# Kernel optimization log

Hardware: AMD Instinct MI355X
Metric: run time of the kernel (lower is better)

Reference implementation:

```python
import jax, jax.numpy as jnp
import numpy as np

# ---- static config (mirrors cfg) ----
B, N, K = 2, 8192, 40
FIRST_DL = 0.03
CONV_RADIUS = 2.5
DEFORM_RADIUS = 5.0
ARCH = ['simple', 'resnetb', 'resnetb_strided', 'resnetb', 'resnetb_strided', 'resnetb', 'nearest_upsample']
SENTINEL = N  # out-of-range support index (torch code uses N_spts_total; here per-batch padded slot count)
GRID = 4096   # voxel hash multiplier; coords stay < GRID for pts in [0,1], dl >= 0.06


def _ball_query_one(q, s, qmask, smask, radius):
    """Radius ball-query: K nearest supports within radius. q:[N,3] s:[M,3]."""
    d2 = jnp.sum((q[:, None, :] - s[None, :, :]) ** 2, axis=-1)          # [N,M]
    d2 = jnp.where(smask[None, :] & (d2 <= radius * radius), d2, jnp.inf)
    vals, idx = jax.lax.top_k(-d2, K)                                     # [N,K]
    idx = jnp.where(jnp.isfinite(vals) & qmask[:, None], idx, SENTINEL)
    return idx.astype(jnp.int32)


ball_query = jax.vmap(_ball_query_one, in_axes=(0, 0, 0, 0, None))


def _grid_subsample_one(pts, mask, dl):
    """Voxel-grid subsampling with unweighted average (padded to N rows)."""
    INT_MAX = jnp.iinfo(jnp.int32).max
    c = jnp.floor(pts / dl).astype(jnp.int32)                             # nonneg for pts in [0,1]
    key_v = (c[:, 0] * GRID + c[:, 1]) * GRID + c[:, 2]
    key_v = jnp.where(mask, key_v, INT_MAX)
    order = jnp.argsort(key_v)
    sk = key_v[order]
    sp = pts[order]
    new = jnp.concatenate([jnp.ones((1,), bool), sk[1:] != sk[:-1]])
    seg = jnp.cumsum(new) - 1                                             # segment id per sorted point
    sums = jax.ops.segment_sum(sp, seg, num_segments=N)                   # [N,3]
    cnt = jax.ops.segment_sum(jnp.ones((N,), pts.dtype), seg, num_segments=N)
    segkey = jax.ops.segment_max(sk, seg, num_segments=N)
    valid = (cnt > 0) & (segkey != INT_MAX)                               # invalid pads sort last
    means = jnp.where(valid[:, None], sums / jnp.maximum(cnt, 1.0)[:, None], 0.0)
    return means, valid, jnp.sum(valid).astype(jnp.int32)


grid_subsample = jax.vmap(_grid_subsample_one, in_axes=(0, 0, None))


def setup_inputs() -> dict:
    key = jax.random.key(0)
    pts = jax.random.uniform(key, (B, N, 3), dtype=jnp.float32)
    return {"pts": pts}


def reference(pts):
    pmask = jnp.ones((B, N), bool)
    lengths = jnp.full((B,), N, jnp.int32)
    points = pts
    r_normal = FIRST_DL * CONV_RADIUS
    layer_blocks = []
    out_points, out_neigh, out_pool, out_up, out_len = [], [], [], [], []
    for bi, block in enumerate(ARCH):
        if 'global' in block or 'upsample' in block:
            break
        if not ('pool' in block or 'strided' in block):
            layer_blocks.append(block)
            if bi < len(ARCH) - 1 and 'upsample' not in ARCH[bi + 1]:
                continue
        if layer_blocks:
            if any('deformable' in b for b in layer_blocks[:-1]):
                r = r_normal * DEFORM_RADIUS / CONV_RADIUS
            else:
                r = r_normal
            conv_i = ball_query(points, points, pmask, pmask, r)
        else:
            conv_i = jnp.full((B, N, K), SENTINEL, jnp.int32)
        if 'pool' in block or 'strided' in block:
            dl = 2 * r_normal / CONV_RADIUS
            pool_p, pool_m, pool_len = grid_subsample(points, pmask, dl)
            r = r_normal * DEFORM_RADIUS / CONV_RADIUS if 'deformable' in block else r_normal
            pool_i = ball_query(pool_p, points, pool_m, pmask, r)
            up_i = ball_query(points, pool_p, pmask, pool_m, 2 * r)
        else:
            pool_i = jnp.full((B, N, K), SENTINEL, jnp.int32)
            up_i = jnp.full((B, N, K), SENTINEL, jnp.int32)
            pool_p = jnp.zeros((B, N, 3), points.dtype)
            pool_m = jnp.zeros((B, N), bool)
            pool_len = jnp.zeros((B,), jnp.int32)
        out_points.append(points)
        out_neigh.append(conv_i)
        out_pool.append(pool_i)
        out_up.append(up_i)
        out_len.append(lengths)
        points, pmask, lengths = pool_p, pool_m, pool_len
        r_normal *= 2
        layer_blocks = []
    return (jnp.stack(out_points),   # [L,B,N,3] padded points per layer
            jnp.stack(out_neigh),    # [L,B,N,K] conv neighbor indices
            jnp.stack(out_pool),     # [L,B,N,K] pooling indices
            jnp.stack(out_up),       # [L,B,N,K] upsampling indices
            jnp.stack(out_len))      # [L,B]     valid lengths
```

## Files before the change

kernel.cpp:

```cpp
#include <hip/hip_runtime.h>

#define BB   2
#define NN   8192
#define KNN  40
#define SENT 8192
#define G0   17
#define G1   9
#define G0_3 (G0*G0*G0)
#define G1_3 (G1*G1*G1)

#define GA   13
#define GB   6
#define GC   3
#define GA_3 (GA*GA*GA)
#define GB_3 (GB*GB*GB)
#define GC_3 (GC*GC*GC)

typedef unsigned long long ull;
typedef unsigned int       u32;
typedef unsigned short     u16;

__device__ __forceinline__ float sqdist(float qx, float qy, float qz,
                                        float sx, float sy, float sz) {
    float dx = __fsub_rn(qx, sx);
    float dy = __fsub_rn(qy, sy);
    float dz = __fsub_rn(qz, sz);
    return __fadd_rn(__fadd_rn(__fmul_rn(dx, dx), __fmul_rn(dy, dy)),
                     __fmul_rn(dz, dz));
}

__device__ __forceinline__ int cell1(float p, float Gf, int G) {
    int c = (int)floorf(__fmul_rn(p, Gf));
    return min(max(c, 0), G - 1);
}
__device__ __forceinline__ int vcell1(float p, float dlf, int G) {
    int c = (int)floorf(__fdiv_rn(p, dlf));
    return min(max(c, 0), G - 1);
}

__device__ __forceinline__ ull shfl_u64(ull x, int src) {
    int lo = __shfl((int)(u32)x, src);
    int hi = __shfl((int)(u32)(x >> 32), src);
    return ((ull)(u32)hi << 32) | (ull)(u32)lo;
}
__device__ __forceinline__ ull shflxor_u64(ull x, int m) {
    int lo = __shfl_xor((int)(u32)x, m);
    int hi = __shfl_xor((int)(u32)(x >> 32), m);
    return ((ull)(u32)hi << 32) | (ull)(u32)lo;
}

__global__ void prep_kernel(const float* __restrict__ pts, float* __restrict__ dout) {
    const size_t PN = (size_t)BB * NN * 3;
    const size_t IN = (size_t)BB * NN * KNN;
    float* out_points0 = dout;
    float* out_pool2   = dout + 3 * PN + 3 * IN + 2 * IN;
    float* out_up2     = dout + 3 * PN + 6 * IN + 2 * IN;
    float* out_len     = dout + 3 * PN + 9 * IN;
    int i = blockIdx.x * 256 + threadIdx.x;
    if (i < (int)PN) out_points0[i] = pts[i];
    if (i < (int)IN) {
        out_pool2[i] = (float)SENT;
        out_up2[i]   = (float)SENT;
    }
    if (i == 0) { out_len[0] = (float)NN; out_len[1] = (float)NN; }
}

__global__ __launch_bounds__(1024) void csr_build(
    const float* __restrict__ pts, const int* __restrict__ len_ptr, int len_const,
    int G, int G3, int* __restrict__ off, int* __restrict__ lst,
    float dlfv, int Gv, int G3v, int* __restrict__ offv, int* __restrict__ rankv,
    int* __restrict__ lstv, int* __restrict__ lenv_dev, float* __restrict__ lenv_out_f) {
    __shared__ int scnt[GA_3];
    __shared__ int soff[GA_3];
    __shared__ int svcnt[G0_3];
    __shared__ int svoff[G0_3];
    __shared__ int wsum[16];
    int b = blockIdx.x;
    int t = threadIdx.x;
    int len = len_ptr ? len_ptr[b] : len_const;
    const float* pb = pts + (size_t)b * NN * 3;
    float Gf = (float)G;
    bool dosub = Gv > 0;
    for (int v = t; v < G3; v += 1024) scnt[v] = 0;
    if (dosub) for (int v = t; v < G3v; v += 1024) svcnt[v] = 0;
    __syncthreads();
    for (int i = t; i < len; i += 1024) {
        float px = pb[i * 3], py = pb[i * 3 + 1], pz = pb[i * 3 + 2];
        int c = (cell1(px, Gf, G) * G + cell1(py, Gf, G)) * G + cell1(pz, Gf, G);
        atomicAdd(&scnt[c], 1);
        if (dosub) {
            int cv = (vcell1(px, dlfv, Gv) * Gv + vcell1(py, dlfv, Gv)) * Gv
                     + vcell1(pz, dlfv, Gv);
            atomicAdd(&svcnt[cv], 1);
        }
    }
    __syncthreads();
    int lane = t & 63, wid = t >> 6;
    {
        int per = (G3 + 1023) >> 10;
        int start = t * per, end = min(start + per, G3);
        if (start > G3) start = G3;
        int csum = 0;
        for (int v = start; v < end; ++v) csum += scnt[v];
        int inc = csum;
        for (int d = 1; d < 64; d <<= 1) {
            int u = __shfl_up(inc, d);
            if (lane >= d) inc += u;
        }
        if (lane == 63) wsum[wid] = inc;
        __syncthreads();
        if (t < 16) {
            int wv = wsum[t];
            for (int d = 1; d < 16; d <<= 1) {
                int u = __shfl_up(wv, d);
                if (t >= d) wv += u;
            }
            wsum[t] = wv;
        }
        __syncthreads();
        int excl = inc - csum + (wid ? wsum[wid - 1] : 0);
        int run = excl;
        int* offb = off + (size_t)b * (G3 + 1);
        for (int v = start; v < end; ++v) {
            soff[v] = run;
            offb[v] = run;
            run += scnt[v];
        }
        if (t == 0) offb[G3] = len;
    }
    __syncthreads();
    if (dosub) {
        int per = (G3v + 1023) >> 10;
        int start = t * per, end = min(start + per, G3v);
        if (start > G3v) start = G3v;
        int ce = 0, co = 0;
        for (int v = start; v < end; ++v) { ce += svcnt[v]; co += (svcnt[v] > 0); }
        int pack = (ce << 14) | co;
        int inc = pack;
        for (int d = 1; d < 64; d <<= 1) {
            int u = __shfl_up(inc, d);
            if (lane >= d) inc += u;
        }
        if (lane == 63) wsum[wid] = inc;
        __syncthreads();
        if (t < 16) {
            int wv = wsum[t];
            for (int d = 1; d < 16; d <<= 1) {
                int u = __shfl_up(wv, d);
                if (t >= d) wv += u;
            }
            wsum[t] = wv;
        }
        __syncthreads();
        int excl = inc - pack + (wid ? wsum[wid - 1] : 0);
        int rune = excl >> 14;
        int runo = excl & 16383;
        int total = wsum[15] & 16383;
        int* offvb  = offv  + (size_t)b * (G3v + 1);
        int* rankvb = rankv + (size_t)b * G3v;
        for (int v = start; v < end; ++v) {
            svoff[v]  = rune;
            offvb[v]  = rune;
            rankvb[v] = runo;
            rune += svcnt[v];
            runo += (svcnt[v] > 0);
        }
        if (t == 0) {
            offvb[G3v] = len;
            lenv_dev[b] = total;
            lenv_out_f[b] = (float)total;
        }
    }
    __syncthreads();
    for (int v = t; v < G3; v += 1024) scnt[v] = 0;
    if (dosub) for (int v = t; v < G3v; v += 1024) svcnt[v] = 0;
    __syncthreads();
    int* lstb = lst + (size_t)b * NN;
    int* lstvb = dosub ? (lstv + (size_t)b * NN) : nullptr;
    for (int i = t; i < len; i += 1024) {
        float px = pb[i * 3], py = pb[i * 3 + 1], pz = pb[i * 3 + 2];
        int c = (cell1(px, Gf, G) * G + cell1(py, Gf, G)) * G + cell1(pz, Gf, G);
        int pos = soff[c] + atomicAdd(&scnt[c], 1);
        lstb[pos] = i;
        if (dosub) {
            int cv = (vcell1(px, dlfv, Gv) * Gv + vcell1(py, dlfv, Gv)) * Gv
                     + vcell1(pz, dlfv, Gv);
            int posv = svoff[cv] + atomicAdd(&svcnt[cv], 1);
            lstvb[posv] = i;
        }
    }
}

__global__ __launch_bounds__(256) void sub_means(
    const float* __restrict__ pts, const int* __restrict__ offg,
    const int* __restrict__ rankg, const int* __restrict__ lst,
    const int* __restrict__ len_dev, int G3, float* __restrict__ out_pts) {
    int b = blockIdx.y;
    int i = blockIdx.x * 256 + threadIdx.x;
    const float* pb = pts + (size_t)b * NN * 3;
    const int* offb  = offg + (size_t)b * (G3 + 1);
    const int* lstb  = lst + (size_t)b * NN;
    if (i < G3) {
        int s = offb[i], e = offb[i + 1];
        int cn = e - s;
        if (cn > 0) {
            float sx = 0.f, sy = 0.f, sz = 0.f;
            int last = -1;
            for (int k = 0; k < cn; ++k) {
                int m = 0x7FFFFFFF;
                for (int j = s; j < e; ++j) {
                    int idx = lstb[j];
                    if (idx > last && idx < m) m = idx;
                }
                sx = __fadd_rn(sx, pb[m * 3]);
                sy = __fadd_rn(sy, pb[m * 3 + 1]);
                sz = __fadd_rn(sz, pb[m * 3 + 2]);
                last = m;
            }
            float rinv = __frcp_rn((float)cn);
            int rk = rankg[(size_t)b * G3 + i];
            float* op = out_pts + ((size_t)b * NN + rk) * 3;
            op[0] = __fmul_rn(sx, rinv);
            op[1] = __fmul_rn(sy, rinv);
            op[2] = __fmul_rn(sz, rinv);
        }
    }
    int total = len_dev[b];
    if (i >= total && i < NN) {
        float* op = out_pts + ((size_t)b * NN + i) * 3;
        op[0] = 0.f; op[1] = 0.f; op[2] = 0.f;
    }
}

struct BqArgs {
    const float* q; const int* qlp; int qlc;
    const float* s; const int* off; const int* lst;
    int G; int G3; float r2; float* out;
};

__global__ __launch_bounds__(256) void bq_wave4(BqArgs pA, BqArgs pB,
                                                BqArgs pC, BqArgs pD) {
    const ull INITK = ~0ull;
    __shared__ ull wlds[4][512];
    int z = blockIdx.z;
    const float* qpts   = z == 0 ? pA.q   : (z == 1 ? pB.q   : (z == 2 ? pC.q   : pD.q));
    const int* qlen_ptr = z == 0 ? pA.qlp : (z == 1 ? pB.qlp : (z == 2 ? pC.qlp : pD.qlp));
    int qlen_const      = z == 0 ? pA.qlc : (z == 1 ? pB.qlc : (z == 2 ? pC.qlc : pD.qlc));
    const float* spts   = z == 0 ? pA.s   : (z == 1 ? pB.s   : (z == 2 ? pC.s   : pD.s));
    const int* off      = z == 0 ? pA.off : (z == 1 ? pB.off : (z == 2 ? pC.off : pD.off));
    const int* lst      = z == 0 ? pA.lst : (z == 1 ? pB.lst : (z == 2 ? pC.lst : pD.lst));
    int G               = z == 0 ? pA.G   : (z == 1 ? pB.G   : (z == 2 ? pC.G   : pD.G));
    int G3              = z == 0 ? pA.G3  : (z == 1 ? pB.G3  : (z == 2 ? pC.G3  : pD.G3));
    float r2            = z == 0 ? pA.r2  : (z == 1 ? pB.r2  : (z == 2 ? pC.r2  : pD.r2));
    float* out          = z == 0 ? pA.out : (z == 1 ? pB.out : (z == 2 ? pC.out : pD.out));

    int t = threadIdx.x;
    int lane = t & 63;
    ull* wl = wlds[t >> 6];
    int b = blockIdx.y;
    int qi = blockIdx.x * 4 + (t >> 6);
    int qlen = qlen_ptr ? qlen_ptr[b] : qlen_const;
    float* op = out + ((size_t)b * NN + qi) * KNN;
    if (qi >= qlen) {
        if (lane < KNN) op[lane] = (float)SENT;
        return;
    }
    const float* qp = qpts + ((size_t)b * NN + qi) * 3;
    float qx = qp[0], qy = qp[1], qz = qp[2];
    float Gf = (float)G;
    int cx = cell1(qx, Gf, G), cy = cell1(qy, Gf, G), cz = cell1(qz, Gf, G);
    const int* offb = off + (size_t)b * (G3 + 1);
    const int* lstb = lst + (size_t)b * NN;
    const float* sp = spts + (size_t)b * NN * 3;

    int cnt = 0, cst = 0;
    if (lane < 27) {
        int dz = lane % 3 - 1, dy = (lane / 3) % 3 - 1, dxx = lane / 9 - 1;
        int x = cx + dxx, y = cy + dy, zz = cz + dz;
        bool ok = ((unsigned)x < (unsigned)G) & ((unsigned)y < (unsigned)G)
                                              & ((unsigned)zz < (unsigned)G);
        int c = ok ? (x * G + y) * G + zz : 0;
        int s = ok ? offb[c] : 0;
        int e = ok ? offb[c + 1] : 0;
        cnt = e - s;
        cst = s;
    }
    int incl = cnt;
#pragma unroll
    for (int d_ = 1; d_ < 64; d_ <<= 1) {
        int u = __shfl_up(incl, d_);
        if (lane >= d_) incl += u;
    }
    int excl = incl - cnt;
    int T = __shfl(incl, 63);

    ull res = INITK;
    bool have_res = false;
    for (int r0 = 0; r0 < T; r0 += 512) {
        ull c0 = INITK, c1 = INITK, c2 = INITK, c3 = INITK,
            c4 = INITK, c5 = INITK, c6 = INITK, c7 = INITK;
#define FILL(S, CS) if (r0 + (S) * 64 < T) {                                   \
            int g = r0 + (S) * 64 + lane;                                      \
            bool gok = g < T;                                                  \
            int gc = gok ? g : (T - 1);                                        \
            int d = 0;                                                         \
            if (__shfl(excl, d | 16) <= gc) d |= 16;                           \
            if (__shfl(excl, d | 8)  <= gc) d |= 8;                            \
            if (__shfl(excl, d | 4)  <= gc) d |= 4;                            \
            if (__shfl(excl, d | 2)  <= gc) d |= 2;                            \
            if (__shfl(excl, d | 1)  <= gc) d |= 1;                            \
            int st = __shfl(cst, d), eg = __shfl(excl, d);                     \
            int idx = lstb[st + (gc - eg)];                                    \
            float sx = sp[idx * 3], sy = sp[idx * 3 + 1], sz = sp[idx * 3 + 2];\
            float d2 = sqdist(qx, qy, qz, sx, sy, sz);                         \
            if (gok && d2 <= r2)                                               \
                CS = (((ull)__float_as_uint(d2)) << 13) | (ull)(u32)idx;       \
        }
        FILL(0, c0) FILL(1, c1) FILL(2, c2) FILL(3, c3)
        FILL(4, c4) FILL(5, c5) FILL(6, c6) FILL(7, c7)
#undef FILL
#define CE(A, B) { ull lo_ = (A < B) ? A : B; ull hi_ = (A < B) ? B : A; A = lo_; B = hi_; }
        CE(c0,c1) CE(c2,c3) CE(c4,c5) CE(c6,c7)
        CE(c0,c2) CE(c1,c3) CE(c4,c6) CE(c5,c7)
        CE(c1,c2) CE(c5,c6)
        CE(c0,c4) CE(c1,c5) CE(c2,c6) CE(c3,c7)
        CE(c2,c4) CE(c3,c5)
        CE(c1,c2) CE(c3,c4) CE(c5,c6)
#undef CE
        int m = (c0 != INITK) + (c1 != INITK) + (c2 != INITK) + (c3 != INITK)
              + (c4 != INITK) + (c5 != INITK) + (c6 != INITK) + (c7 != INITK);
        int incm = m;
#pragma unroll
        for (int d_ = 1; d_ < 64; d_ <<= 1) {
            int u = __shfl_up(incm, d_);
            if (lane >= d_) incm += u;
        }
        int base = incm - m;
        int M = __shfl(incm, 63);
        asm volatile("s_waitcnt lgkmcnt(0)" ::: "memory");
        __builtin_amdgcn_sched_barrier(0);
        if (m > 0) {
            wl[base] = c0;
            if (m > 1) wl[base + 1] = c1;
            if (m > 2) wl[base + 2] = c2;
            if (m > 3) wl[base + 3] = c3;
            if (m > 4) wl[base + 4] = c4;
            if (m > 5) wl[base + 5] = c5;
            if (m > 6) wl[base + 6] = c6;
            if (m > 7) wl[base + 7] = c7;
        }
        asm volatile("s_waitcnt lgkmcnt(0)" ::: "memory");
        __builtin_amdgcn_sched_barrier(0);
        int npass = (M + 63) >> 6;
        for (int p = 0; p < npass; ++p) {
            int D = p * 64 + lane;
            ull key = (D < M) ? wl[D] : INITK;
#pragma unroll
            for (int k = 2; k <= 64; k <<= 1) {
#pragma unroll
                for (int jj = k >> 1; jj > 0; jj >>= 1) {
                    ull other = shflxor_u64(key, jj);
                    bool up = ((lane & k) == 0);
                    bool lowlane = ((lane & jj) == 0);
                    bool takeMin = (lowlane == up);
                    bool lt = key < other;
                    key = (takeMin == lt) ? key : other;
                }
            }
            if (!have_res) {
                res = key;
                have_res = true;
            } else {
                ull rb = shfl_u64(key, 63 - lane);
                ull lo_ = (res < rb) ? res : rb;
#pragma unroll
                for (int jj = 32; jj > 0; jj >>= 1) {
                    ull other = shflxor_u64(lo_, jj);
                    bool lowlane = ((lane & jj) == 0);
                    bool lt = lo_ < other;
                    lo_ = (lowlane == lt) ? lo_ : other;
                }
                res = lo_;
            }
        }
    }
    if (lane < KNN)
        op[lane] = (res == INITK) ? (float)SENT : (float)(int)(res & 0x1FFFu);
}

extern "C" void kernel_launch(void* const* d_in, const int* in_sizes, int n_in,
                              void* d_out, int out_size, void* d_ws, size_t ws_size,
                              hipStream_t stream) {
    const float* pts = (const float*)d_in[0];
    float* dout = (float*)d_out;
    const size_t PN = (size_t)BB * NN * 3;
    const size_t IN = (size_t)BB * NN * KNN;
    float* out_points = dout;
    float* out_neigh  = dout + 3 * PN;
    float* out_pool   = out_neigh + 3 * IN;
    float* out_up     = out_pool + 3 * IN;
    float* out_len    = out_up + 3 * IN;
    float* pts1 = out_points + PN;
    float* pts2 = out_points + 2 * PN;

    int*   len1  = (int*)d_ws;
    int*   len2  = len1 + BB;
    int*   offV0 = len2 + BB;
    int*   rnk0  = offV0 + (size_t)BB * (G0_3 + 1);
    int*   lstV0 = rnk0 + (size_t)BB * G0_3;
    int*   offV1 = lstV0 + (size_t)BB * NN;
    int*   rnk1  = offV1 + (size_t)BB * (G1_3 + 1);
    int*   lstV1 = rnk1 + (size_t)BB * G1_3;
    int*   offA  = lstV1 + (size_t)BB * NN;
    int*   lstA  = offA + (size_t)BB * (GA_3 + 1);
    int*   offB  = lstA + (size_t)BB * NN;
    int*   lstB  = offB + (size_t)BB * (GB_3 + 1);
    int*   offC  = lstB + (size_t)BB * NN;
    int*   lstC  = offC + (size_t)BB * (GC_3 + 1);

    double r_normal = 0.03 * 2.5;
    double r0 = r_normal;
    double dl0 = 2.0 * r_normal / 2.5;
    float r2_0   = (float)(r0 * r0);
    float r2_up0 = (float)((2.0 * r0) * (2.0 * r0));
    float dlf0   = (float)dl0;
    r_normal *= 2.0;
    double r1 = r_normal;
    double dl1 = 2.0 * r_normal / 2.5;
    float r2_1   = (float)(r1 * r1);
    float r2_up1 = (float)((2.0 * r1) * (2.0 * r1));
    float dlf1   = (float)dl1;
    r_normal *= 2.0;
    float r2_2 = (float)(r_normal * r_normal);

    BqArgs conv0 = { pts,  nullptr, NN, pts,  offA, lstA, GA, GA_3, r2_0,   out_neigh + 0 * IN };
    BqArgs pool0 = { pts1, len1,    0,  pts,  offA, lstA, GA, GA_3, r2_0,   out_pool  + 0 * IN };
    BqArgs up0   = { pts,  nullptr, NN, pts1, offB, lstB, GB, GB_3, r2_up0, out_up    + 0 * IN };
    BqArgs conv1 = { pts1, len1,    0,  pts1, offB, lstB, GB, GB_3, r2_1,   out_neigh + 1 * IN };
    BqArgs pool1 = { pts2, len2,    0,  pts1, offB, lstB, GB, GB_3, r2_1,   out_pool  + 1 * IN };
    BqArgs up1   = { pts1, len1,    0,  pts2, offC, lstC, GC, GC_3, r2_up1, out_up    + 1 * IN };
    BqArgs conv2 = { pts2, len2,    0,  pts2, offC, lstC, GC, GC_3, r2_2,   out_neigh + 2 * IN };

    dim3 qgrid3(NN / 4, BB, 3);
    dim3 qgrid4(NN / 4, BB, 4);
    dim3 mgrid(NN / 256, BB);

    prep_kernel<<<(int)((IN + 255) / 256), 256, 0, stream>>>(pts, dout);
    csr_build<<<BB, 1024, 0, stream>>>(pts, nullptr, NN, GA, GA_3, offA, lstA,
                                       dlf0, G0, G0_3, offV0, rnk0, lstV0,
                                       len1, out_len + 2);
    sub_means<<<mgrid, 256, 0, stream>>>(pts, offV0, rnk0, lstV0, len1, G0_3, pts1);
    csr_build<<<BB, 1024, 0, stream>>>(pts1, len1, 0, GB, GB_3, offB, lstB,
                                       dlf1, G1, G1_3, offV1, rnk1, lstV1,
                                       len2, out_len + 4);
    sub_means<<<mgrid, 256, 0, stream>>>(pts1, offV1, rnk1, lstV1, len2, G1_3, pts2);
    csr_build<<<BB, 1024, 0, stream>>>(pts2, len2, 0, GC, GC_3, offC, lstC,
                                       0.f, 0, 0, nullptr, nullptr, nullptr,
                                       nullptr, nullptr);
    bq_wave4<<<qgrid3, 256, 0, stream>>>(conv0, pool0, up0, up0);
    bq_wave4<<<qgrid4, 256, 0, stream>>>(conv1, pool1, up1, conv2);
}
```

Measured before the change: 195.9 us.

## Store cell-sorted support coords with indices as float4 and skip redundant sort stage

```diff
diff --git a/kernel.cpp b/kernel.cpp
--- a/kernel.cpp
+++ b/kernel.cpp
@@ -67,7 +67,7 @@
 
 __global__ __launch_bounds__(1024) void csr_build(
     const float* __restrict__ pts, const int* __restrict__ len_ptr, int len_const,
-    int G, int G3, int* __restrict__ off, int* __restrict__ lst,
+    int G, int G3, int* __restrict__ off, float4* __restrict__ lst4,
     float dlfv, int Gv, int G3v, int* __restrict__ offv, int* __restrict__ rankv,
     int* __restrict__ lstv, int* __restrict__ lenv_dev, float* __restrict__ lenv_out_f) {
     __shared__ int scnt[GA_3];
@@ -175,13 +175,13 @@
     for (int v = t; v < G3; v += 1024) scnt[v] = 0;
     if (dosub) for (int v = t; v < G3v; v += 1024) svcnt[v] = 0;
     __syncthreads();
-    int* lstb = lst + (size_t)b * NN;
+    float4* lst4b = lst4 + (size_t)b * NN;
     int* lstvb = dosub ? (lstv + (size_t)b * NN) : nullptr;
     for (int i = t; i < len; i += 1024) {
         float px = pb[i * 3], py = pb[i * 3 + 1], pz = pb[i * 3 + 2];
         int c = (cell1(px, Gf, G) * G + cell1(py, Gf, G)) * G + cell1(pz, Gf, G);
         int pos = soff[c] + atomicAdd(&scnt[c], 1);
-        lstb[pos] = i;
+        lst4b[pos] = make_float4(px, py, pz, __int_as_float(i));
         if (dosub) {
             int cv = (vcell1(px, dlfv, Gv) * Gv + vcell1(py, dlfv, Gv)) * Gv
                      + vcell1(pz, dlfv, Gv);
@@ -234,7 +234,7 @@
 
 struct BqArgs {
     const float* q; const int* qlp; int qlc;
-    const float* s; const int* off; const int* lst;
+    const float4* lst; const int* off;
     int G; int G3; float r2; float* out;
 };
 
@@ -246,9 +246,8 @@
     const float* qpts   = z == 0 ? pA.q   : (z == 1 ? pB.q   : (z == 2 ? pC.q   : pD.q));
     const int* qlen_ptr = z == 0 ? pA.qlp : (z == 1 ? pB.qlp : (z == 2 ? pC.qlp : pD.qlp));
     int qlen_const      = z == 0 ? pA.qlc : (z == 1 ? pB.qlc : (z == 2 ? pC.qlc : pD.qlc));
-    const float* spts   = z == 0 ? pA.s   : (z == 1 ? pB.s   : (z == 2 ? pC.s   : pD.s));
+    const float4* lst   = z == 0 ? pA.lst : (z == 1 ? pB.lst : (z == 2 ? pC.lst : pD.lst));
     const int* off      = z == 0 ? pA.off : (z == 1 ? pB.off : (z == 2 ? pC.off : pD.off));
-    const int* lst      = z == 0 ? pA.lst : (z == 1 ? pB.lst : (z == 2 ? pC.lst : pD.lst));
     int G               = z == 0 ? pA.G   : (z == 1 ? pB.G   : (z == 2 ? pC.G   : pD.G));
     int G3              = z == 0 ? pA.G3  : (z == 1 ? pB.G3  : (z == 2 ? pC.G3  : pD.G3));
     float r2            = z == 0 ? pA.r2  : (z == 1 ? pB.r2  : (z == 2 ? pC.r2  : pD.r2));
@@ -270,8 +269,7 @@
     float Gf = (float)G;
     int cx = cell1(qx, Gf, G), cy = cell1(qy, Gf, G), cz = cell1(qz, Gf, G);
     const int* offb = off + (size_t)b * (G3 + 1);
-    const int* lstb = lst + (size_t)b * NN;
-    const float* sp = spts + (size_t)b * NN * 3;
+    const float4* lstb = lst + (size_t)b * NN;
 
     int cnt = 0, cst = 0;
     if (lane < 27) {
@@ -310,11 +308,11 @@
             if (__shfl(excl, d | 2)  <= gc) d |= 2;                            \
             if (__shfl(excl, d | 1)  <= gc) d |= 1;                            \
             int st = __shfl(cst, d), eg = __shfl(excl, d);                     \
-            int idx = lstb[st + (gc - eg)];                                    \
-            float sx = sp[idx * 3], sy = sp[idx * 3 + 1], sz = sp[idx * 3 + 2];\
-            float d2 = sqdist(qx, qy, qz, sx, sy, sz);                         \
+            float4 f = lstb[st + (gc - eg)];                                   \
+            float d2 = sqdist(qx, qy, qz, f.x, f.y, f.z);                      \
             if (gok && d2 <= r2)                                               \
-                CS = (((ull)__float_as_uint(d2)) << 13) | (ull)(u32)idx;       \
+                CS = (((ull)__float_as_uint(d2)) << 13)                        \
+                     | (ull)(u32)__float_as_int(f.w);                          \
         }
         FILL(0, c0) FILL(1, c1) FILL(2, c2) FILL(3, c3)
         FILL(4, c4) FILL(5, c5) FILL(6, c6) FILL(7, c7)
@@ -355,8 +353,9 @@
         for (int p = 0; p < npass; ++p) {
             int D = p * 64 + lane;
             ull key = (D < M) ? wl[D] : INITK;
-#pragma unroll
-            for (int k = 2; k <= 64; k <<= 1) {
+            int mc = M - p * 64;
+#pragma unroll
+            for (int k = 2; k <= 32; k <<= 1) {
 #pragma unroll
                 for (int jj = k >> 1; jj > 0; jj >>= 1) {
                     ull other = shflxor_u64(key, jj);
@@ -365,6 +364,15 @@
                     bool takeMin = (lowlane == up);
                     bool lt = key < other;
                     key = (takeMin == lt) ? key : other;
+                }
+            }
+            if (mc > 32) {
+#pragma unroll
+                for (int jj = 32; jj > 0; jj >>= 1) {
+                    ull other = shflxor_u64(key, jj);
+                    bool lowlane = ((lane & jj) == 0);
+                    bool lt = key < other;
+                    key = (lowlane == lt) ? key : other;
                 }
             }
             if (!have_res) {
@@ -403,7 +411,10 @@
     float* pts1 = out_points + PN;
     float* pts2 = out_points + 2 * PN;
 
-    int*   len1  = (int*)d_ws;
+    float4* lst4A = (float4*)d_ws;
+    float4* lst4B = lst4A + (size_t)BB * NN;
+    float4* lst4C = lst4B + (size_t)BB * NN;
+    int*   len1  = (int*)(lst4C + (size_t)BB * NN);
     int*   len2  = len1 + BB;
     int*   offV0 = len2 + BB;
     int*   rnk0  = offV0 + (size_t)BB * (G0_3 + 1);
@@ -412,11 +423,8 @@
     int*   rnk1  = offV1 + (size_t)BB * (G1_3 + 1);
     int*   lstV1 = rnk1 + (size_t)BB * G1_3;
     int*   offA  = lstV1 + (size_t)BB * NN;
-    int*   lstA  = offA + (size_t)BB * (GA_3 + 1);
-    int*   offB  = lstA + (size_t)BB * NN;
-    int*   lstB  = offB + (size_t)BB * (GB_3 + 1);
-    int*   offC  = lstB + (size_t)BB * NN;
-    int*   lstC  = offC + (size_t)BB * (GC_3 + 1);
+    int*   offB  = offA + (size_t)BB * (GA_3 + 1);
+    int*   offC  = offB + (size_t)BB * (GB_3 + 1);
 
     double r_normal = 0.03 * 2.5;
     double r0 = r_normal;
@@ -433,28 +441,28 @@
     r_normal *= 2.0;
     float r2_2 = (float)(r_normal * r_normal);
 
-    BqArgs conv0 = { pts,  nullptr, NN, pts,  offA, lstA, GA, GA_3, r2_0,   out_neigh + 0 * IN };
-    BqArgs pool0 = { pts1, len1,    0,  pts,  offA, lstA, GA, GA_3, r2_0,   out_pool  + 0 * IN };
-    BqArgs up0   = { pts,  nullptr, NN, pts1, offB, lstB, GB, GB_3, r2_up0, out_up    + 0 * IN };
-    BqArgs conv1 = { pts1, len1,    0,  pts1, offB, lstB, GB, GB_3, r2_1,   out_neigh + 1 * IN };
-    BqArgs pool1 = { pts2, len2,    0,  pts1, offB, lstB, GB, GB_3, r2_1,   out_pool  + 1 * IN };
-    BqArgs up1   = { pts1, len1,    0,  pts2, offC, lstC, GC, GC_3, r2_up1, out_up    + 1 * IN };
-    BqArgs conv2 = { pts2, len2,    0,  pts2, offC, lstC, GC, GC_3, r2_2,   out_neigh + 2 * IN };
+    BqArgs conv0 = { pts,  nullptr, NN, lst4A, offA, GA, GA_3, r2_0,   out_neigh + 0 * IN };
+    BqArgs pool0 = { pts1, len1,    0,  lst4A, offA, GA, GA_3, r2_0,   out_pool  + 0 * IN };
+    BqArgs up0   = { pts,  nullptr, NN, lst4B, offB, GB, GB_3, r2_up0, out_up    + 0 * IN };
+    BqArgs conv1 = { pts1, len1,    0,  lst4B, offB, GB, GB_3, r2_1,   out_neigh + 1 * IN };
+    BqArgs pool1 = { pts2, len2,    0,  lst4B, offB, GB, GB_3, r2_1,   out_pool  + 1 * IN };
+    BqArgs up1   = { pts1, len1,    0,  lst4C, offC, GC, GC_3, r2_up1, out_up    + 1 * IN };
+    BqArgs conv2 = { pts2, len2,    0,  lst4C, offC, GC, GC_3, r2_2,   out_neigh + 2 * IN };
 
     dim3 qgrid3(NN / 4, BB, 3);
     dim3 qgrid4(NN / 4, BB, 4);
     dim3 mgrid(NN / 256, BB);
 
     prep_kernel<<<(int)((IN + 255) / 256), 256, 0, stream>>>(pts, dout);
-    csr_build<<<BB, 1024, 0, stream>>>(pts, nullptr, NN, GA, GA_3, offA, lstA,
+    csr_build<<<BB, 1024, 0, stream>>>(pts, nullptr, NN, GA, GA_3, offA, lst4A,
                                        dlf0, G0, G0_3, offV0, rnk0, lstV0,
                                        len1, out_len + 2);
     sub_means<<<mgrid, 256, 0, stream>>>(pts, offV0, rnk0, lstV0, len1, G0_3, pts1);
-    csr_build<<<BB, 1024, 0, stream>>>(pts1, len1, 0, GB, GB_3, offB, lstB,
+    csr_build<<<BB, 1024, 0, stream>>>(pts1, len1, 0, GB, GB_3, offB, lst4B,
                                        dlf1, G1, G1_3, offV1, rnk1, lstV1,
                                        len2, out_len + 4);
     sub_means<<<mgrid, 256, 0, stream>>>(pts1, offV1, rnk1, lstV1, len2, G1_3, pts2);
-    csr_build<<<BB, 1024, 0, stream>>>(pts2, len2, 0, GC, GC_3, offC, lstC,
+    csr_build<<<BB, 1024, 0, stream>>>(pts2, len2, 0, GC, GC_3, offC, lst4C,
                                        0.f, 0, 0, nullptr, nullptr, nullptr,
                                        nullptr, nullptr);
     bq_wave4<<<qgrid3, 256, 0, stream>>>(conv0, pool0, up0, up0);
```

Measured after the change: 189.3 us. -3.4%, faster.
